# Optimization experiments

Measured on AMD Instinct MI355X. Metric: run time of the kernel, lower is better.

Reference implementation:

```python
import jax, jax.numpy as jnp
import numpy as np

B, T, I, H, O = 64, 256, 256, 1024, 256


def _lstm_cell(x, h, c, W_ih, W_hh, b_ih, b_hh):
    # PyTorch LSTMCell: gates = x@W_ih^T + b_ih + h@W_hh^T + b_hh, chunked as i,f,g,o
    gates = x @ W_ih.T + h @ W_hh.T + (b_ih + b_hh)
    i_g, f_g, g_g, o_g = jnp.split(gates, 4, axis=-1)
    c_new = jax.nn.sigmoid(f_g) * c + jax.nn.sigmoid(i_g) * jnp.tanh(g_g)
    h_new = jax.nn.sigmoid(o_g) * jnp.tanh(c_new)
    return h_new, c_new


def setup_inputs() -> dict:
    key = jax.random.key(0)
    ks = jax.random.split(key, 11)
    s1 = 1.0 / np.sqrt(H)
    return {
        "x": jax.random.normal(ks[0], (B, T, I), dtype=jnp.float32),
        "W_ih1": jax.random.uniform(ks[1], (4 * H, I), jnp.float32, -s1, s1),
        "W_hh1": jax.random.uniform(ks[2], (4 * H, H), jnp.float32, -s1, s1),
        "b_ih1": jax.random.uniform(ks[3], (4 * H,), jnp.float32, -s1, s1),
        "b_hh1": jax.random.uniform(ks[4], (4 * H,), jnp.float32, -s1, s1),
        "W_ih2": jax.random.uniform(ks[5], (4 * H, I + H), jnp.float32, -s1, s1),
        "W_hh2": jax.random.uniform(ks[6], (4 * H, H), jnp.float32, -s1, s1),
        "b_ih2": jax.random.uniform(ks[7], (4 * H,), jnp.float32, -s1, s1),
        "b_hh2": jax.random.uniform(ks[8], (4 * H,), jnp.float32, -s1, s1),
        "W_l": jax.random.uniform(ks[9], (O, I + H), jnp.float32, -s1, s1),
        "b_l": jax.random.uniform(ks[10], (O,), jnp.float32, -s1, s1),
    }


def reference(x, W_ih1, W_hh1, b_ih1, b_hh1, W_ih2, W_hh2, b_ih2, b_hh2, W_l, b_l):
    batch = x.shape[0]
    zeros = jnp.zeros((batch, H), dtype=x.dtype)
    init = (zeros, zeros, zeros, zeros)  # h1, c1, h2, c2

    def step(carry, x_t):
        h1, c1, h2, c2 = carry
        h1, c1 = _lstm_cell(x_t, h1, c1, W_ih1, W_hh1, b_ih1, b_hh1)
        x2 = jnp.concatenate([x_t, h1], axis=1)  # [B, I+H]
        h2, c2 = _lstm_cell(x2, h2, c2, W_ih2, W_hh2, b_ih2, b_hh2)
        x3 = jnp.concatenate([x_t, h2], axis=1)  # [B, I+H]
        y_t = x3 @ W_l.T + b_l  # [B, O]
        return (h1, c1, h2, c2), y_t

    xs = jnp.swapaxes(x, 0, 1)  # [T, B, I]
    _, ys = jax.lax.scan(step, init, xs)  # ys: [T, B, O]
    return jnp.swapaxes(ys, 0, 1)  # [B, T, O]
```

## Files before the change

### kernel.cpp

```cpp
#include <hip/hip_runtime.h>


typedef __attribute__((ext_vector_type(8))) short short8;
typedef __attribute__((ext_vector_type(16))) float f32x16;
typedef __attribute__((ext_vector_type(4))) float f32x4;

#define Tn 256
#define In 256
#define Hn 1024
#define On 256
#define SP 136
#define NL1 64
#define NL2 128
#define NY  16
#define NBLK (NL1 + NL2 + NY)
#define CHUNK_B 17408
#define SMEM_SZ 55808
#define BHe 65536
#define RELEASE_IDX 240

#define WS_WIH1 0
#define WS_WHH1 2097152
#define WS_WIH2 10485760
#define WS_WHH2 20971520
#define WS_WL   29360128
#define WS_X    30015488
#define WS_H1   38404096
#define WS_H2   38666240
#define WS_ARR  38928384

#define WAIT_LGKM0() __builtin_amdgcn_s_waitcnt(0xC07F)
#define RAW_BARRIER() do { \
    WAIT_LGKM0(); \
    __builtin_amdgcn_sched_barrier(0); \
    __builtin_amdgcn_s_barrier(); \
    __builtin_amdgcn_sched_barrier(0); \
  } while (0)

#define STAGE_WAIT2(rem) do { \
    __builtin_amdgcn_sched_barrier(0); \
    if ((rem) >= 3)      asm volatile("s_waitcnt vmcnt(6)" ::: "memory"); \
    else if ((rem) == 2) asm volatile("s_waitcnt vmcnt(4)" ::: "memory"); \
    else if ((rem) == 1) asm volatile("s_waitcnt vmcnt(2)" ::: "memory"); \
    else                 asm volatile("s_waitcnt vmcnt(0)" ::: "memory"); \
    __builtin_amdgcn_sched_barrier(0); \
  } while (0)

#define STAGE_WAIT4(rem) do { \
    __builtin_amdgcn_sched_barrier(0); \
    if ((rem) >= 3)      asm volatile("s_waitcnt vmcnt(12)" ::: "memory"); \
    else if ((rem) == 2) asm volatile("s_waitcnt vmcnt(8)"  ::: "memory"); \
    else if ((rem) == 1) asm volatile("s_waitcnt vmcnt(4)"  ::: "memory"); \
    else                 asm volatile("s_waitcnt vmcnt(0)"  ::: "memory"); \
    __builtin_amdgcn_sched_barrier(0); \
  } while (0)

#define GLD16(dst, ptr) \
  asm volatile("global_load_dwordx4 %0, %1, off" : "=v"(dst) : "v"(ptr))
#define GLD16C(dst, ptr) \
  asm volatile("global_load_dwordx4 %0, %1, off sc1" : "=v"(dst) : "v"(ptr))

static __device__ __forceinline__ unsigned short f2b(float f) {
  union { float f; unsigned int i; } v; v.f = f;
  unsigned int u = v.i;
  return (unsigned short)((u + 0x7FFFu + ((u >> 16) & 1u)) >> 16);
}
static __device__ __forceinline__ float sigm(float x) { return 1.0f / (1.0f + __expf(-x)); }
static __device__ __forceinline__ float tanhf_(float x) {
  float ax = fabsf(x);
  float e = __expf(-2.0f * ax);
  return copysignf((1.0f - e) / (1.0f + e), x);
}
static __device__ __forceinline__ int ld32a(const void* p) {
  return __hip_atomic_load((const int*)p, __ATOMIC_RELAXED, __HIP_MEMORY_SCOPE_AGENT);
}
static __device__ __forceinline__ void st32a(void* p, unsigned int v) {
  __hip_atomic_store((unsigned int*)p, v, __ATOMIC_RELAXED, __HIP_MEMORY_SCOPE_AGENT);
}
static __device__ __forceinline__ void st64a(void* p, unsigned long long v) {
  __hip_atomic_store((unsigned long long*)p, v, __ATOMIC_RELAXED, __HIP_MEMORY_SCOPE_AGENT);
}

static __device__ __forceinline__ void grid_barrier(int* arrive, int bid, int tid,
                                                    int lane, int tgt) {
  __syncthreads();
  if (tid == 0)
    st32a(&arrive[bid], (unsigned int)tgt);
  if (bid == 0) {
    if (tid < 64) {
      bool done = false;
      while (!done) {
        bool ok = true;
        #pragma unroll
        for (int j = 0; j < 4; ++j) {
          int idx = lane + j * 64;
          if (idx < NBLK) {
            int v = ld32a(&arrive[idx]);
            ok = ok && (v >= tgt);
          }
        }
        done = __all(ok);
        if (!done) __builtin_amdgcn_s_sleep(1);
      }
      if (tid == 0)
        st32a(&arrive[RELEASE_IDX], (unsigned int)tgt);
    }
    __syncthreads();
  } else {
    if (tid == 0) {
      while (ld32a(&arrive[RELEASE_IDX]) < tgt) __builtin_amdgcn_s_sleep(1);
    }
    __syncthreads();
  }
}

__global__ void __launch_bounds__(256) cvt_bf16(const float* __restrict__ src,
                                                unsigned short* __restrict__ dst, int n4) {
  int i = blockIdx.x * blockDim.x + threadIdx.x;
  if (i >= n4) return;
  float4 v = ((const float4*)src)[i];
  ushort4 o;
  o.x = f2b(v.x); o.y = f2b(v.y); o.z = f2b(v.z); o.w = f2b(v.w);
  ((ushort4*)dst)[i] = o;
}

__global__ void __launch_bounds__(256) prep_zero(unsigned short* h1buf,
                                                 unsigned short* h2buf,
                                                 int* arrive) {
  int i = blockIdx.x * blockDim.x + threadIdx.x;
  st64a((unsigned long long*)h1buf + i, 0ull);
  st64a((unsigned long long*)h1buf + 16384 + i, 0ull);
  st64a((unsigned long long*)h2buf + i, 0ull);
  st64a((unsigned long long*)h2buf + 16384 + i, 0ull);
  if (i < 256) st32a(arrive + i, 0u);
}

__global__ void __launch_bounds__(256, 1) lstm_persist(
    const unsigned short* __restrict__ x,
    const unsigned short* __restrict__ Wih1, const unsigned short* __restrict__ Whh1,
    const float* __restrict__ bih1, const float* __restrict__ bhh1,
    const unsigned short* __restrict__ Wih2, const unsigned short* __restrict__ Whh2,
    const float* __restrict__ bih2, const float* __restrict__ bhh2,
    const unsigned short* __restrict__ Wl,  const float* __restrict__ bl,
    float* __restrict__ out,
    unsigned short* __restrict__ h1buf, unsigned short* __restrict__ h2buf,
    int* __restrict__ arrive)
{
  extern __shared__ char smem[];
  unsigned short* sbuf0 = (unsigned short*)smem;
  unsigned short* sbuf1 = (unsigned short*)(smem + CHUNK_B);
  float* sG = (float*)(smem + 2 * CHUNK_B);
  float* sc = (float*)(smem + 2 * CHUNK_B + 16896);

  const int tid = threadIdx.x;
  const int bid = blockIdx.x;
  const int lane = tid & 63;
  const int wid = tid >> 6;
  const int r0  = tid >> 4;
  const int sg  = tid & 15;
  const int l31 = lane & 31;
  const int hi8 = (lane >> 5) << 3;

  for (int e = tid; e < 1024; e += 256) sc[e] = 0.0f;

  if (bid < NL1) {
    const int bh = bid & 1;
    const int rb = bh << 5;
    const int j0 = (bid >> 1) << 5;
    const int gr = wid * 1024 + j0 + l31;

    uint4 rs[4][2];

    short8 w[80];
    #pragma unroll
    for (int c = 0; c < 10; ++c) {
      const unsigned short* wrow = (c < 2) ? (Wih1 + (size_t)gr * In + c * 128)
                                           : (Whh1 + (size_t)gr * Hn + (c - 2) * 128);
      #pragma unroll
      for (int k8 = 0; k8 < 8; ++k8)
        w[c * 8 + k8] = *(const short8*)(wrow + k8 * 16 + hi8);
    }
    float bs[4][4];
    {
      int op4 = (tid & 7) << 2;
      #pragma unroll
      for (int k = 0; k < 4; ++k) {
        int o = op4 + k;
        #pragma unroll
        for (int g = 0; g < 4; ++g)
          bs[k][g] = bih1[g * 1024 + j0 + o] + bhh1[g * 1024 + j0 + o];
      }
    }

    for (int s = 0; s < Tn; ++s) {
      const int t = s;
      const unsigned short* h1rd = h1buf + ((t + 1) & 1) * BHe;
      unsigned short* h1wr = h1buf + (t & 1) * BHe;
      f32x16 acc0 = {}, acc1 = {};

      auto ldc = [&](int cc, int d) {
        if (cc < 2) {
          const char* p = (const char*)(x + ((size_t)(rb + r0) * Tn + t) * In + cc * 128 + sg * 8);
          GLD16(rs[d][0], p);
          GLD16(rs[d][1], p + 16 * Tn * In * 2);
        } else {
          const char* p = (const char*)(h1rd + (size_t)(rb + r0) * Hn + (cc - 2) * 128 + sg * 8);
          GLD16C(rs[d][0], p);
          GLD16C(rs[d][1], p + 16 * Hn * 2);
        }
      };
      ldc(0, 0); ldc(1, 1); ldc(2, 2); ldc(3, 3);

      #pragma unroll
      for (int c = 0; c < 10; ++c) {
        unsigned short* buf = (c & 1) ? sbuf1 : sbuf0;
        STAGE_WAIT2(9 - c);
        {
          unsigned short* db = buf + r0 * SP + sg * 8;
          *(uint4*)db = rs[c & 3][0];
          *(uint4*)(db + 16 * SP) = rs[c & 3][1];
        }
        if (c + 4 < 10) ldc(c + 4, c & 3);
        RAW_BARRIER();
        const unsigned short* ab = buf + l31 * SP + hi8;
        #pragma unroll
        for (int k8 = 0; k8 < 8; k8 += 2) {
          acc0 = __builtin_amdgcn_mfma_f32_32x32x16_bf16(*(const short8*)(ab + k8 * 16),      w[c * 8 + k8],     acc0, 0, 0, 0);
          acc1 = __builtin_amdgcn_mfma_f32_32x32x16_bf16(*(const short8*)(ab + k8 * 16 + 16), w[c * 8 + k8 + 1], acc1, 0, 0, 0);
        }
      }
      RAW_BARRIER();

      f32x16 accv = acc0 + acc1;
      #pragma unroll
      for (int i = 0; i < 16; ++i) {
        int rm = (i & 3) + ((i >> 2) << 3) + ((lane >> 5) << 2);
        sG[wid * 1056 + rm * 33 + l31] = accv[i];
      }
      __syncthreads();

      {
        int b = tid >> 3, op4 = (tid & 7) << 2;
        unsigned int pk0 = 0, pk1 = 0;
        #pragma unroll
        for (int k = 0; k < 4; ++k) {
          int o = op4 + k, e = b * 32 + o;
          float ig = sG[       b * 33 + o] + bs[k][0];
          float fg = sG[1056 + b * 33 + o] + bs[k][1];
          float gg = sG[2112 + b * 33 + o] + bs[k][2];
          float og = sG[3168 + b * 33 + o] + bs[k][3];
          float cn = sigm(fg) * sc[e] + sigm(ig) * tanhf_(gg);
          sc[e] = cn;
          unsigned int hb = f2b(sigm(og) * tanhf_(cn));
          if (k < 2) pk0 |= hb << (16 * k); else pk1 |= hb << (16 * (k - 2));
        }
        st64a(h1wr + (size_t)(rb + b) * Hn + j0 + op4,
              ((unsigned long long)pk1 << 32) | pk0);
      }
      grid_barrier(arrive, bid, tid, lane, s + 1);
    }
    grid_barrier(arrive, bid, tid, lane, Tn + 1);

  } else if (bid < NL1 + NL2) {
    const int lb = bid - NL1;
    const int bh = lb & 1;
    const int rb = bh << 5;
    const int j0 = (lb >> 1) << 4;
    const int ntile = wid & 1, ks = wid >> 1;
    const int grow = ntile * 32 + l31;
    const int gr = ((grow >> 4) << 10) + j0 + (grow & 15);

    uint4 rs[4][2];

    short8 w[72];
    if (ks == 0) {
      #pragma unroll
      for (int c = 0; c < 9; ++c)
        #pragma unroll
        for (int k8 = 0; k8 < 8; ++k8)
          w[c * 8 + k8] = *(const short8*)(Wih2 + (size_t)gr * 1280 + c * 128 + k8 * 16 + hi8);
    } else {
      #pragma unroll
      for (int c = 0; c < 9; ++c) {
        const unsigned short* wrow = (c == 0) ? (Wih2 + (size_t)gr * 1280 + 1152)
                                              : (Whh2 + (size_t)gr * Hn + (c - 1) * 128);
        #pragma unroll
        for (int k8 = 0; k8 < 8; ++k8)
          w[c * 8 + k8] = *(const short8*)(wrow + k8 * 16 + hi8);
      }
    }
    float bs[2][4];
    {
      int op2 = (tid & 7) << 1;
      #pragma unroll
      for (int k = 0; k < 2; ++k) {
        int o = op2 + k;
        #pragma unroll
        for (int g = 0; g < 4; ++g)
          bs[k][g] = bih2[g * 1024 + j0 + o] + bhh2[g * 1024 + j0 + o];
      }
    }

    grid_barrier(arrive, bid, tid, lane, 1);

    for (int s = 1; s <= Tn; ++s) {
      const int t = s - 1;
      const unsigned short* h1rd = h1buf + (t & 1) * BHe;
      const unsigned short* h2rd = h2buf + ((t + 1) & 1) * BHe;
      unsigned short* h2wr = h2buf + (t & 1) * BHe;
      f32x16 acc0 = {}, acc1 = {};

      auto ldc = [&](int cc, int d) {
        if (cc < 2) {
          const char* p = (const char*)(x + ((size_t)(rb + r0) * Tn + t) * In + cc * 128 + sg * 8);
          GLD16(rs[d][0], p);
          GLD16(rs[d][1], p + 16 * Tn * In * 2);
        } else {
          const unsigned short* src = (cc < 10) ? (h1rd + (cc - 2) * 128)
                                                : (h2rd + (cc - 10) * 128);
          const char* p = (const char*)(src + (size_t)(rb + r0) * Hn + sg * 8);
          GLD16C(rs[d][0], p);
          GLD16C(rs[d][1], p + 16 * Hn * 2);
        }
      };
      ldc(0, 0); ldc(1, 1); ldc(2, 2); ldc(3, 3);

      #pragma unroll
      for (int c = 0; c < 18; ++c) {
        unsigned short* buf = (c & 1) ? sbuf1 : sbuf0;
        STAGE_WAIT2(17 - c);
        {
          unsigned short* db = buf + r0 * SP + sg * 8;
          *(uint4*)db = rs[c & 3][0];
          *(uint4*)(db + 16 * SP) = rs[c & 3][1];
        }
        if (c + 4 < 18) ldc(c + 4, c & 3);
        RAW_BARRIER();
        bool active = (ks == 0) ? (c < 9) : (c >= 9);
        if (active) {
          int ib = ((ks == 0) ? c : (c - 9)) * 8;
          const unsigned short* ab = buf + l31 * SP + hi8;
          #pragma unroll
          for (int k8 = 0; k8 < 8; k8 += 2) {
            acc0 = __builtin_amdgcn_mfma_f32_32x32x16_bf16(*(const short8*)(ab + k8 * 16),      w[ib + k8],     acc0, 0, 0, 0);
            acc1 = __builtin_amdgcn_mfma_f32_32x32x16_bf16(*(const short8*)(ab + k8 * 16 + 16), w[ib + k8 + 1], acc1, 0, 0, 0);
          }
        }
      }
      RAW_BARRIER();

      f32x16 accv = acc0 + acc1;
      #pragma unroll
      for (int i = 0; i < 16; ++i) {
        int rm = (i & 3) + ((i >> 2) << 3) + ((lane >> 5) << 2);
        sG[ks * 2112 + grow * 33 + rm] = accv[i];
      }
      __syncthreads();

      {
        int b = tid >> 3, op2 = (tid & 7) << 1;
        unsigned int pack = 0;
        #pragma unroll
        for (int k = 0; k < 2; ++k) {
          int o = op2 + k, e = b * 16 + o;
          float ig = sG[(     o) * 33 + b] + sG[2112 + (     o) * 33 + b] + bs[k][0];
          float fg = sG[(16 + o) * 33 + b] + sG[2112 + (16 + o) * 33 + b] + bs[k][1];
          float gg = sG[(32 + o) * 33 + b] + sG[2112 + (32 + o) * 33 + b] + bs[k][2];
          float og = sG[(48 + o) * 33 + b] + sG[2112 + (48 + o) * 33 + b] + bs[k][3];
          float cn = sigm(fg) * sc[e] + sigm(ig) * tanhf_(gg);
          sc[e] = cn;
          pack |= ((unsigned int)f2b(sigm(og) * tanhf_(cn))) << (16 * k);
        }
        st32a(h2wr + (size_t)(rb + b) * Hn + j0 + op2, pack);
      }
      grid_barrier(arrive, bid, tid, lane, s + 1);
    }

  } else {
    const int o0 = (bid - NL1 - NL2) << 4;
    const int quad = lane >> 4;
    const int l15 = lane & 15;
    const int hi8y = quad << 3;

    uint4 rs[4][4];

    short8 wy[40];
    #pragma unroll
    for (int c = 0; c < 10; ++c)
      #pragma unroll
      for (int q = 0; q < 4; ++q)
        wy[c * 4 + q] = *(const short8*)(Wl + (size_t)(o0 + l15) * 1280 + c * 128 + q * 32 + hi8y);
    const float blv = bl[o0 + l15];

    grid_barrier(arrive, bid, tid, lane, 1);
    grid_barrier(arrive, bid, tid, lane, 2);

    for (int s = 2; s <= Tn + 1; ++s) {
      const int t = s - 2;
      const unsigned short* h2rd = h2buf + (t & 1) * BHe;
      f32x4 acc0 = {}, acc1 = {};

      auto ldc = [&](int cc, int d) {
        if (cc < 2) {
          const char* p = (const char*)(x + ((size_t)r0 * Tn + t) * In + cc * 128 + sg * 8);
          #pragma unroll
          for (int j = 0; j < 4; ++j) GLD16(rs[d][j], p + (size_t)j * (16 * Tn * In * 2));
        } else {
          const char* p = (const char*)(h2rd + (size_t)r0 * Hn + (cc - 2) * 128 + sg * 8);
          #pragma unroll
          for (int j = 0; j < 4; ++j) GLD16C(rs[d][j], p + j * (16 * Hn * 2));
        }
      };
      ldc(0, 0); ldc(1, 1); ldc(2, 2); ldc(3, 3);

      #pragma unroll
      for (int c = 0; c < 10; ++c) {
        unsigned short* buf = (c & 1) ? sbuf1 : sbuf0;
        STAGE_WAIT4(9 - c);
        {
          unsigned short* db = buf + r0 * SP + sg * 8;
          #pragma unroll
          for (int j = 0; j < 4; ++j) *(uint4*)(db + j * (16 * SP)) = rs[c & 3][j];
        }
        if (c + 4 < 10) ldc(c + 4, c & 3);
        RAW_BARRIER();
        const unsigned short* ab = buf + (wid * 16 + l15) * SP + hi8y;
        acc0 = __builtin_amdgcn_mfma_f32_16x16x32_bf16(*(const short8*)(ab),      wy[c * 4 + 0], acc0, 0, 0, 0);
        acc1 = __builtin_amdgcn_mfma_f32_16x16x32_bf16(*(const short8*)(ab + 32), wy[c * 4 + 1], acc1, 0, 0, 0);
        acc0 = __builtin_amdgcn_mfma_f32_16x16x32_bf16(*(const short8*)(ab + 64), wy[c * 4 + 2], acc0, 0, 0, 0);
        acc1 = __builtin_amdgcn_mfma_f32_16x16x32_bf16(*(const short8*)(ab + 96), wy[c * 4 + 3], acc1, 0, 0, 0);
      }
      RAW_BARRIER();

      f32x4 accv = acc0 + acc1;
      #pragma unroll
      for (int i = 0; i < 4; ++i) {
        int b = wid * 16 + quad * 4 + i;
        out[((size_t)b * Tn + t) * On + o0 + l15] = accv[i] + blv;
      }
      if (s <= Tn) grid_barrier(arrive, bid, tid, lane, s + 1);
    }
  }
}

extern "C" void kernel_launch(void* const* d_in, const int* in_sizes, int n_in,
                              void* d_out, int out_size, void* d_ws, size_t ws_size,
                              hipStream_t stream) {
  (void)in_sizes; (void)n_in; (void)out_size; (void)ws_size;
  const float* xf    = (const float*)d_in[0];
  const float* Wih1f = (const float*)d_in[1];
  const float* Whh1f = (const float*)d_in[2];
  const float* bih1  = (const float*)d_in[3];
  const float* bhh1  = (const float*)d_in[4];
  const float* Wih2f = (const float*)d_in[5];
  const float* Whh2f = (const float*)d_in[6];
  const float* bih2  = (const float*)d_in[7];
  const float* bhh2  = (const float*)d_in[8];
  const float* Wlf   = (const float*)d_in[9];
  const float* bl    = (const float*)d_in[10];
  float* out = (float*)d_out;

  char* ws = (char*)d_ws;
  unsigned short* Wih1b = (unsigned short*)(ws + WS_WIH1);
  unsigned short* Whh1b = (unsigned short*)(ws + WS_WHH1);
  unsigned short* Wih2b = (unsigned short*)(ws + WS_WIH2);
  unsigned short* Whh2b = (unsigned short*)(ws + WS_WHH2);
  unsigned short* Wlb   = (unsigned short*)(ws + WS_WL);
  unsigned short* xb    = (unsigned short*)(ws + WS_X);
  unsigned short* h1buf = (unsigned short*)(ws + WS_H1);
  unsigned short* h2buf = (unsigned short*)(ws + WS_H2);
  int* arrive           = (int*)(ws + WS_ARR);

  hipLaunchKernelGGL(cvt_bf16, dim3(1024), dim3(256), 0, stream, Wih1f, Wih1b, 262144);
  hipLaunchKernelGGL(cvt_bf16, dim3(4096), dim3(256), 0, stream, Whh1f, Whh1b, 1048576);
  hipLaunchKernelGGL(cvt_bf16, dim3(5120), dim3(256), 0, stream, Wih2f, Wih2b, 1310720);
  hipLaunchKernelGGL(cvt_bf16, dim3(4096), dim3(256), 0, stream, Whh2f, Whh2b, 1048576);
  hipLaunchKernelGGL(cvt_bf16, dim3(320),  dim3(256), 0, stream, Wlf,   Wlb,   81920);
  hipLaunchKernelGGL(cvt_bf16, dim3(4096), dim3(256), 0, stream, xf,    xb,    1048576);

  hipLaunchKernelGGL(prep_zero, dim3(64), dim3(256), 0, stream, h1buf, h2buf, arrive);

  hipLaunchKernelGGL(lstm_persist, dim3(NBLK), dim3(256), SMEM_SZ, stream,
                     xb, Wih1b, Whh1b, bih1, bhh1, Wih2b, Whh2b, bih2, bhh2, Wlb, bl,
                     out, h1buf, h2buf, arrive);
}
```

Baseline: 2.150 ms.

## Split grid barrier and overlap x-projection with barrier wait in LSTM layers

The grid barrier is split into a publish step and a wait step. The LSTM layer blocks now prefetch the next timestep's x and compute its input-projection MFMAs before waiting for the release, which takes that work off the serial critical path. Staging moves from 128-wide to 256-wide chunks (LSP stride) with a 3-deep register ring, so each timestep has fewer chunk/barrier iterations. The layer-2 split-K partition is changed so one half covers x plus h1 and the other covers h2, and the master barrier block moves to the last block. In exchange, the x prefetch registers stay live across the elementwise phase and the barrier wait, which raises register pressure.

Measured after the change: 1.923 ms. 1.12x faster.

```diff
diff --git a/kernel.cpp b/kernel.cpp
--- a/kernel.cpp
+++ b/kernel.cpp
@@ -10,10 +10,12 @@
 #define Hn 1024
 #define On 256
 #define SP 136
+#define LSP 264
 #define NL1 64
 #define NL2 128
 #define NY  16
 #define NBLK (NL1 + NL2 + NY)
+#define MASTER_BID (NBLK - 1)
 #define CHUNK_B 17408
 #define SMEM_SZ 55808
 #define BHe 65536
@@ -37,12 +39,9 @@
     __builtin_amdgcn_sched_barrier(0); \
   } while (0)
 
-#define STAGE_WAIT2(rem) do { \
+#define STWAIT_N(n) do { \
     __builtin_amdgcn_sched_barrier(0); \
-    if ((rem) >= 3)      asm volatile("s_waitcnt vmcnt(6)" ::: "memory"); \
-    else if ((rem) == 2) asm volatile("s_waitcnt vmcnt(4)" ::: "memory"); \
-    else if ((rem) == 1) asm volatile("s_waitcnt vmcnt(2)" ::: "memory"); \
-    else                 asm volatile("s_waitcnt vmcnt(0)" ::: "memory"); \
+    asm volatile("s_waitcnt vmcnt(" n ")" ::: "memory"); \
     __builtin_amdgcn_sched_barrier(0); \
   } while (0)
 
@@ -81,12 +80,14 @@
   __hip_atomic_store((unsigned long long*)p, v, __ATOMIC_RELAXED, __HIP_MEMORY_SCOPE_AGENT);
 }
 
-static __device__ __forceinline__ void grid_barrier(int* arrive, int bid, int tid,
-                                                    int lane, int tgt) {
+static __device__ __forceinline__ void publish_arrive(int* arrive, int bid, int tid, int tgt) {
   __syncthreads();
   if (tid == 0)
     st32a(&arrive[bid], (unsigned int)tgt);
-  if (bid == 0) {
+}
+static __device__ __forceinline__ void wait_release(int* arrive, int bid, int tid,
+                                                    int lane, int tgt) {
+  if (bid == MASTER_BID) {
     if (tid < 64) {
       bool done = false;
       while (!done) {
@@ -105,13 +106,12 @@
       if (tid == 0)
         st32a(&arrive[RELEASE_IDX], (unsigned int)tgt);
     }
-    __syncthreads();
   } else {
     if (tid == 0) {
       while (ld32a(&arrive[RELEASE_IDX]) < tgt) __builtin_amdgcn_s_sleep(1);
     }
-    __syncthreads();
   }
+  __syncthreads();
 }
 
 __global__ void __launch_bounds__(256) cvt_bf16(const float* __restrict__ src,
@@ -156,10 +156,12 @@
   const int bid = blockIdx.x;
   const int lane = tid & 63;
   const int wid = tid >> 6;
-  const int r0  = tid >> 4;
-  const int sg  = tid & 15;
   const int l31 = lane & 31;
   const int hi8 = (lane >> 5) << 3;
+  const int rbase = tid >> 5;
+  const int sl = tid & 31;
+  const int r0h = tid >> 4;
+  const int sgh = tid & 15;
 
   for (int e = tid; e < 1024; e += 256) sc[e] = 0.0f;
 
@@ -169,7 +171,7 @@
     const int j0 = (bid >> 1) << 5;
     const int gr = wid * 1024 + j0 + l31;
 
-    uint4 rs[4][2];
+    uint4 rs[3][4];
 
     short8 w[80];
     #pragma unroll
@@ -192,42 +194,62 @@
       }
     }
 
+    auto ld_x = [&](int t, int d) {
+      const char* p = (const char*)(x + ((size_t)(rb + rbase) * Tn + t) * In) + sl * 16;
+      #pragma unroll
+      for (int j = 0; j < 4; ++j) GLD16(rs[d][j], p + (size_t)j * (8 * Tn * In * 2));
+    };
+
+    ld_x(0, 0);
+
     for (int s = 0; s < Tn; ++s) {
       const int t = s;
       const unsigned short* h1rd = h1buf + ((t + 1) & 1) * BHe;
       unsigned short* h1wr = h1buf + (t & 1) * BHe;
       f32x16 acc0 = {}, acc1 = {};
 
-      auto ldc = [&](int cc, int d) {
-        if (cc < 2) {
-          const char* p = (const char*)(x + ((size_t)(rb + r0) * Tn + t) * In + cc * 128 + sg * 8);
-          GLD16(rs[d][0], p);
-          GLD16(rs[d][1], p + 16 * Tn * In * 2);
-        } else {
-          const char* p = (const char*)(h1rd + (size_t)(rb + r0) * Hn + (cc - 2) * 128 + sg * 8);
-          GLD16C(rs[d][0], p);
-          GLD16C(rs[d][1], p + 16 * Hn * 2);
-        }
-      };
-      ldc(0, 0); ldc(1, 1); ldc(2, 2); ldc(3, 3);
-
-      #pragma unroll
-      for (int c = 0; c < 10; ++c) {
+      auto ld_h1 = [&](int cc, int d) {
+        const char* p = (const char*)(h1rd + (size_t)(rb + rbase) * Hn + (cc - 1) * 256) + sl * 16;
+        #pragma unroll
+        for (int j = 0; j < 4; ++j) GLD16C(rs[d][j], p + j * (8 * Hn * 2));
+      };
+      auto stage = [&](unsigned short* buf, int d) {
+        unsigned short* db = buf + rbase * LSP + sl * 8;
+        #pragma unroll
+        for (int j = 0; j < 4; ++j) *(uint4*)(db + j * (8 * LSP)) = rs[d][j];
+      };
+      auto mfmaC = [&](const unsigned short* buf, int sc2) {
+        #pragma unroll
+        for (int h = 0; h < 2; ++h) {
+          const unsigned short* ab = buf + l31 * LSP + h * 128 + hi8;
+          const int ib = (sc2 + h) * 8;
+          #pragma unroll
+          for (int k8 = 0; k8 < 8; k8 += 2) {
+            acc0 = __builtin_amdgcn_mfma_f32_32x32x16_bf16(*(const short8*)(ab + k8 * 16),      w[ib + k8],     acc0, 0, 0, 0);
+            acc1 = __builtin_amdgcn_mfma_f32_32x32x16_bf16(*(const short8*)(ab + k8 * 16 + 16), w[ib + k8 + 1], acc1, 0, 0, 0);
+          }
+        }
+      };
+
+      STWAIT_N("0");
+      stage(sbuf0, 0);
+      RAW_BARRIER();
+      mfmaC(sbuf0, 0);
+
+      wait_release(arrive, bid, tid, lane, s);
+
+      ld_h1(1, 1); ld_h1(2, 2); ld_h1(3, 0);
+
+      #pragma unroll
+      for (int c = 1; c <= 4; ++c) {
         unsigned short* buf = (c & 1) ? sbuf1 : sbuf0;
-        STAGE_WAIT2(9 - c);
-        {
-          unsigned short* db = buf + r0 * SP + sg * 8;
-          *(uint4*)db = rs[c & 3][0];
-          *(uint4*)(db + 16 * SP) = rs[c & 3][1];
-        }
-        if (c + 4 < 10) ldc(c + 4, c & 3);
+        if (c <= 2)      STWAIT_N("8");
+        else if (c == 3) STWAIT_N("4");
+        else             STWAIT_N("0");
+        stage(buf, c % 3);
+        if (c + 3 <= 4) ld_h1(c + 3, (c + 3) % 3);
         RAW_BARRIER();
-        const unsigned short* ab = buf + l31 * SP + hi8;
-        #pragma unroll
-        for (int k8 = 0; k8 < 8; k8 += 2) {
-          acc0 = __builtin_amdgcn_mfma_f32_32x32x16_bf16(*(const short8*)(ab + k8 * 16),      w[c * 8 + k8],     acc0, 0, 0, 0);
-          acc1 = __builtin_amdgcn_mfma_f32_32x32x16_bf16(*(const short8*)(ab + k8 * 16 + 16), w[c * 8 + k8 + 1], acc1, 0, 0, 0);
-        }
+        mfmaC(buf, 2 * c);
       }
       RAW_BARRIER();
 
@@ -238,6 +260,8 @@
         sG[wid * 1056 + rm * 33 + l31] = accv[i];
       }
       __syncthreads();
+
+      if (s + 1 < Tn) ld_x(s + 1, 0);
 
       {
         int b = tid >> 3, op4 = (tid & 7) << 2;
@@ -257,9 +281,9 @@
         st64a(h1wr + (size_t)(rb + b) * Hn + j0 + op4,
               ((unsigned long long)pk1 << 32) | pk0);
       }
-      grid_barrier(arrive, bid, tid, lane, s + 1);
-    }
-    grid_barrier(arrive, bid, tid, lane, Tn + 1);
+      publish_arrive(arrive, bid, tid, s + 1);
+    }
+    publish_arrive(arrive, bid, tid, Tn + 1);
 
   } else if (bid < NL1 + NL2) {
     const int lb = bid - NL1;
@@ -270,24 +294,21 @@
     const int grow = ntile * 32 + l31;
     const int gr = ((grow >> 4) << 10) + j0 + (grow & 15);
 
-    uint4 rs[4][2];
-
-    short8 w[72];
+    uint4 rs[3][4];
+
+    short8 w[80];
     if (ks == 0) {
       #pragma unroll
-      for (int c = 0; c < 9; ++c)
+      for (int c = 0; c < 10; ++c)
         #pragma unroll
         for (int k8 = 0; k8 < 8; ++k8)
           w[c * 8 + k8] = *(const short8*)(Wih2 + (size_t)gr * 1280 + c * 128 + k8 * 16 + hi8);
     } else {
       #pragma unroll
-      for (int c = 0; c < 9; ++c) {
-        const unsigned short* wrow = (c == 0) ? (Wih2 + (size_t)gr * 1280 + 1152)
-                                              : (Whh2 + (size_t)gr * Hn + (c - 1) * 128);
+      for (int c = 0; c < 8; ++c)
         #pragma unroll
         for (int k8 = 0; k8 < 8; ++k8)
-          w[c * 8 + k8] = *(const short8*)(wrow + k8 * 16 + hi8);
-      }
+          w[c * 8 + k8] = *(const short8*)(Whh2 + (size_t)gr * Hn + c * 128 + k8 * 16 + hi8);
     }
     float bs[2][4];
     {
@@ -301,7 +322,14 @@
       }
     }
 
-    grid_barrier(arrive, bid, tid, lane, 1);
+    auto ld_x2 = [&](int t, int d) {
+      const char* p = (const char*)(x + ((size_t)(rb + rbase) * Tn + t) * In) + sl * 16;
+      #pragma unroll
+      for (int j = 0; j < 4; ++j) GLD16(rs[d][j], p + (size_t)j * (8 * Tn * In * 2));
+    };
+
+    ld_x2(0, 0);
+    publish_arrive(arrive, bid, tid, 1);
 
     for (int s = 1; s <= Tn; ++s) {
       const int t = s - 1;
@@ -310,42 +338,53 @@
       unsigned short* h2wr = h2buf + (t & 1) * BHe;
       f32x16 acc0 = {}, acc1 = {};
 
-      auto ldc = [&](int cc, int d) {
-        if (cc < 2) {
-          const char* p = (const char*)(x + ((size_t)(rb + r0) * Tn + t) * In + cc * 128 + sg * 8);
-          GLD16(rs[d][0], p);
-          GLD16(rs[d][1], p + 16 * Tn * In * 2);
-        } else {
-          const unsigned short* src = (cc < 10) ? (h1rd + (cc - 2) * 128)
-                                                : (h2rd + (cc - 10) * 128);
-          const char* p = (const char*)(src + (size_t)(rb + r0) * Hn + sg * 8);
-          GLD16C(rs[d][0], p);
-          GLD16C(rs[d][1], p + 16 * Hn * 2);
-        }
-      };
-      ldc(0, 0); ldc(1, 1); ldc(2, 2); ldc(3, 3);
-
-      #pragma unroll
-      for (int c = 0; c < 18; ++c) {
-        unsigned short* buf = (c & 1) ? sbuf1 : sbuf0;
-        STAGE_WAIT2(17 - c);
-        {
-          unsigned short* db = buf + r0 * SP + sg * 8;
-          *(uint4*)db = rs[c & 3][0];
-          *(uint4*)(db + 16 * SP) = rs[c & 3][1];
-        }
-        if (c + 4 < 18) ldc(c + 4, c & 3);
-        RAW_BARRIER();
-        bool active = (ks == 0) ? (c < 9) : (c >= 9);
-        if (active) {
-          int ib = ((ks == 0) ? c : (c - 9)) * 8;
-          const unsigned short* ab = buf + l31 * SP + hi8;
+      auto ld_hc = [&](int cc, int d) {
+        const unsigned short* src = (cc < 5) ? (h1rd + (cc - 1) * 256)
+                                             : (h2rd + (cc - 5) * 256);
+        const char* p = (const char*)(src + (size_t)(rb + rbase) * Hn) + sl * 16;
+        #pragma unroll
+        for (int j = 0; j < 4; ++j) GLD16C(rs[d][j], p + j * (8 * Hn * 2));
+      };
+      auto stage = [&](unsigned short* buf, int d) {
+        unsigned short* db = buf + rbase * LSP + sl * 8;
+        #pragma unroll
+        for (int j = 0; j < 4; ++j) *(uint4*)(db + j * (8 * LSP)) = rs[d][j];
+      };
+      auto mfmaC2 = [&](const unsigned short* buf, int c) {
+        bool active = (ks == 0) ? (c < 5) : (c >= 5);
+        if (!active) return;
+        const int sc2 = (ks == 0) ? (2 * c) : (2 * (c - 5));
+        #pragma unroll
+        for (int h = 0; h < 2; ++h) {
+          const unsigned short* ab = buf + l31 * LSP + h * 128 + hi8;
+          const int ib = (sc2 + h) * 8;
           #pragma unroll
           for (int k8 = 0; k8 < 8; k8 += 2) {
             acc0 = __builtin_amdgcn_mfma_f32_32x32x16_bf16(*(const short8*)(ab + k8 * 16),      w[ib + k8],     acc0, 0, 0, 0);
             acc1 = __builtin_amdgcn_mfma_f32_32x32x16_bf16(*(const short8*)(ab + k8 * 16 + 16), w[ib + k8 + 1], acc1, 0, 0, 0);
           }
         }
+      };
+
+      STWAIT_N("0");
+      stage(sbuf0, 0);
+      RAW_BARRIER();
+      mfmaC2(sbuf0, 0);
+
+      wait_release(arrive, bid, tid, lane, s);
+
+      ld_hc(1, 1); ld_hc(2, 2); ld_hc(3, 0);
+
+      #pragma unroll
+      for (int c = 1; c <= 8; ++c) {
+        unsigned short* buf = (c & 1) ? sbuf1 : sbuf0;
+        if (c <= 6)      STWAIT_N("8");
+        else if (c == 7) STWAIT_N("4");
+        else             STWAIT_N("0");
+        stage(buf, c % 3);
+        if (c + 3 <= 8) ld_hc(c + 3, (c + 3) % 3);
+        RAW_BARRIER();
+        mfmaC2(buf, c);
       }
       RAW_BARRIER();
 
@@ -356,6 +395,8 @@
         sG[ks * 2112 + grow * 33 + rm] = accv[i];
       }
       __syncthreads();
+
+      if (s < Tn) ld_x2(t + 1, 0);
 
       {
         int b = tid >> 3, op2 = (tid & 7) << 1;
@@ -373,7 +414,7 @@
         }
         st32a(h2wr + (size_t)(rb + b) * Hn + j0 + op2, pack);
       }
-      grid_barrier(arrive, bid, tid, lane, s + 1);
+      publish_arrive(arrive, bid, tid, s + 1);
     }
 
   } else {
@@ -392,8 +433,10 @@
         wy[c * 4 + q] = *(const short8*)(Wl + (size_t)(o0 + l15) * 1280 + c * 128 + q * 32 + hi8y);
     const float blv = bl[o0 + l15];
 
-    grid_barrier(arrive, bid, tid, lane, 1);
-    grid_barrier(arrive, bid, tid, lane, 2);
+    publish_arrive(arrive, bid, tid, 1);
+    wait_release(arrive, bid, tid, lane, 1);
+    publish_arrive(arrive, bid, tid, 2);
+    wait_release(arrive, bid, tid, lane, 2);
 
     for (int s = 2; s <= Tn + 1; ++s) {
       const int t = s - 2;
@@ -402,11 +445,11 @@
 
       auto ldc = [&](int cc, int d) {
         if (cc < 2) {
-          const char* p = (const char*)(x + ((size_t)r0 * Tn + t) * In + cc * 128 + sg * 8);
+          const char* p = (const char*)(x + ((size_t)r0h * Tn + t) * In + cc * 128 + sgh * 8);
           #pragma unroll
           for (int j = 0; j < 4; ++j) GLD16(rs[d][j], p + (size_t)j * (16 * Tn * In * 2));
         } else {
-          const char* p = (const char*)(h2rd + (size_t)r0 * Hn + (cc - 2) * 128 + sg * 8);
+          const char* p = (const char*)(h2rd + (size_t)r0h * Hn + (cc - 2) * 128 + sgh * 8);
           #pragma unroll
           for (int j = 0; j < 4; ++j) GLD16C(rs[d][j], p + j * (16 * Hn * 2));
         }
@@ -418,7 +461,7 @@
         unsigned short* buf = (c & 1) ? sbuf1 : sbuf0;
         STAGE_WAIT4(9 - c);
         {
-          unsigned short* db = buf + r0 * SP + sg * 8;
+          unsigned short* db = buf + r0h * SP + sgh * 8;
           #pragma unroll
           for (int j = 0; j < 4; ++j) *(uint4*)(db + j * (16 * SP)) = rs[c & 3][j];
         }
@@ -438,7 +481,10 @@
         int b = wid * 16 + quad * 4 + i;
         out[((size_t)b * Tn + t) * On + o0 + l15] = accv[i] + blv;
       }
-      if (s <= Tn) grid_barrier(arrive, bid, tid, lane, s + 1);
+      if (s <= Tn) {
+        publish_arrive(arrive, bid, tid, s + 1);
+        wait_release(arrive, bid, tid, lane, s + 1);
+      }
     }
   }
 }
```
